# Performance work log

Hardware: AMD Instinct MI355X
Metric: run time of the kernel (lower is better)

## Reference

```python
import jax, jax.numpy as jnp
import numpy as np

N, E, IN, H0, H1 = 50000, 1600000, 64, 64, 128


def _gcn(h, W, b, row, col):
    # PyG GCNConv, add_self_loops=False, unit edge weights:
    # out[col] += d^{-1/2}[row] * d^{-1/2}[col] * (h @ W)[row]; bias added after aggregation
    n = h.shape[0]
    deg = jnp.zeros((n,), h.dtype).at[col].add(jnp.ones((row.shape[0],), h.dtype))
    dinv = jnp.where(deg > 0, jax.lax.rsqrt(jnp.maximum(deg, 1e-12)), 0.0)
    norm = (dinv[row] * dinv[col])[:, None]  # [E,1]
    m = h @ W  # transform before propagate (small GEMM)
    out = jnp.zeros((n, W.shape[1]), h.dtype).at[col].add(norm * m[row])
    return out + b


def _bn(h, g, b):
    # BatchNorm1d training-mode math (biased variance), eps=1e-5
    mu = h.mean(0)
    var = ((h - mu) ** 2).mean(0)
    return g * (h - mu) * jax.lax.rsqrt(var + 1e-5) + b


def _san(h):
    return jnp.nan_to_num(h, nan=0.0, posinf=100.0, neginf=-100.0)


def _slice(x, ei, W0, b0, W1, b1, res1, g0, be0, g1, be1):
    row, col = ei[0], ei[1]
    # layer 0: conv -> bn -> relu -> (dropout=eval identity) -> residual (Identity, 64==64) -> nan_to_num
    h1 = _san(jax.nn.relu(_bn(_gcn(x, W0, b0, row, col), g0, be0)) + x)
    # layer 1 (last): conv -> bn -> residual (Linear proj 64->128, no bias) -> nan_to_num
    h2 = _san(_bn(_gcn(h1, W1, b1, row, col), g1, be1) + h1 @ res1)
    return h2


def setup_inputs() -> dict:
    k = jax.random.split(jax.random.key(0), 16)
    f = lambda kk, sh, s: jax.random.normal(kk, sh, jnp.float32) * s
    return {
        "x": f(k[0], (N, IN), 1.0),
        "edge_index0": jax.random.randint(k[1], (2, E), 0, N),
        "edge_index1": jax.random.randint(k[2], (2, E), 0, N),
        "w0_s0": f(k[3], (IN, H0), 0.1), "b0_s0": jnp.zeros((H0,), jnp.float32),
        "w1_s0": f(k[4], (H0, H1), 0.1), "b1_s0": jnp.zeros((H1,), jnp.float32),
        "res1_s0": f(k[5], (H0, H1), 0.1),
        "w0_s1": f(k[6], (IN, H0), 0.1), "b0_s1": jnp.zeros((H0,), jnp.float32),
        "w1_s1": f(k[7], (H0, H1), 0.1), "b1_s1": jnp.zeros((H1,), jnp.float32),
        "res1_s1": f(k[8], (H0, H1), 0.1),
        "bn_g0": jnp.ones((H0,), jnp.float32), "bn_b0": jnp.zeros((H0,), jnp.float32),
        "bn_g1": jnp.ones((H1,), jnp.float32), "bn_b1": jnp.zeros((H1,), jnp.float32),
        "fc1_w": f(k[9], (2 * H1, H1), 0.1), "fc1_b": jnp.zeros((H1,), jnp.float32),
        "fc2_w": f(k[10], (H1, 2), 0.1), "fc2_b": jnp.zeros((2,), jnp.float32),
    }


def reference(x, edge_index0, edge_index1,
              w0_s0, b0_s0, w1_s0, b1_s0, res1_s0,
              w0_s1, b0_s1, w1_s1, b1_s1, res1_s1,
              bn_g0, bn_b0, bn_g1, bn_b1,
              fc1_w, fc1_b, fc2_w, fc2_b):
    out0 = _slice(x, edge_index0, w0_s0, b0_s0, w1_s0, b1_s0, res1_s0, bn_g0, bn_b0, bn_g1, bn_b1)
    out1 = _slice(x, edge_index1, w0_s1, b0_s1, w1_s1, b1_s1, res1_s1, bn_g0, bn_b0, bn_g1, bn_b1)
    combined = jnp.concatenate([out0, out1], axis=1)  # [N, 2*H1]
    h = jax.nn.relu(combined @ fc1_w + fc1_b)  # dropout is eval-mode identity
    logits = h @ fc2_w + fc2_b
    return logits, jax.nn.softmax(logits, axis=1)
```

## Files before the change

### kernel.cpp

```cpp
#include <hip/hip_runtime.h>
#include <hip/hip_bf16.h>
#include <math.h>


typedef short v8s __attribute__((ext_vector_type(8)));
typedef float f32x4 __attribute__((ext_vector_type(4)));

#define BSTRIDE 10240

__device__ __forceinline__ float sanf(float v) {
    if (v != v) return 0.f;
    if (isinf(v)) return v > 0.f ? 100.f : -100.f;
    return v;
}

__device__ __forceinline__ unsigned short bf16of(float v) {
    __hip_bfloat16 h = __float2bfloat16(v);
    return *(unsigned short*)&h;
}
__device__ __forceinline__ unsigned pack2(float lo, float hi) {
    return (unsigned)bf16of(lo) | ((unsigned)bf16of(hi) << 16);
}
__device__ __forceinline__ float uflo(unsigned u) { return __uint_as_float(u << 16); }
__device__ __forceinline__ float ufhi(unsigned u) { return __uint_as_float(u & 0xFFFF0000u); }
__device__ __forceinline__ float fofbf16(unsigned short u) {
    return __uint_as_float(((unsigned)u) << 16);
}

__device__ __forceinline__ void packone(const float* __restrict__ src, unsigned* __restrict__ dst,
                                        int L, int Khalf, int F) {
    int c = L / Khalf, kp = L - c * Khalf;
    dst[L] = pack2(src[(2 * kp) * F + c], src[(2 * kp + 1) * F + c]);
}

__global__ __launch_bounds__(256) void prep_kernel(const float* __restrict__ w0_0,
                                                   const float* __restrict__ w0_1,
                                                   const float* __restrict__ w1_0,
                                                   const float* __restrict__ w1_1,
                                                   const float* __restrict__ r_0,
                                                   const float* __restrict__ r_1,
                                                   const float* __restrict__ fc1,
                                                   unsigned* __restrict__ wpk,
                                                   int* __restrict__ bcnt,
                                                   float* __restrict__ sums) {
    int gid = blockIdx.x * 256 + threadIdx.x;
    if (gid < 512) bcnt[gid] = 0;
    if (gid < 8192) sums[gid] = 0.f;
    if (gid < 2048)       packone(w0_0, wpk + 0,     gid - 0,     32, 64);
    else if (gid < 4096)  packone(w0_1, wpk + 2048,  gid - 2048,  32, 64);
    else if (gid < 8192)  packone(w1_0, wpk + 4096,  gid - 4096,  32, 128);
    else if (gid < 12288) packone(w1_1, wpk + 8192,  gid - 8192,  32, 128);
    else if (gid < 16384) packone(r_0,  wpk + 12288, gid - 12288, 32, 128);
    else if (gid < 20480) packone(r_1,  wpk + 16384, gid - 16384, 32, 128);
    else if (gid < 36864) packone(fc1,  wpk + 20480, gid - 20480, 128, 128);
}


__global__ __launch_bounds__(512) void kC_bin(const int* __restrict__ ei0,
                                              const int* __restrict__ ei1,
                                              int* __restrict__ bcnt,
                                              unsigned* __restrict__ binned,
                                              int E, int n) {
    __shared__ int cnt[512];
    __shared__ int base[512];
    int t = threadIdx.x;
    cnt[t] = 0;
    int E2 = 2 * E;
    int e0 = blockIdx.x * 8192;
    unsigned pk[16];
    int bk[16];
    __syncthreads();
#pragma unroll
    for (int j = 0; j < 16; ++j) {
        int ge = e0 + t + j * 512;
        bk[j] = -1;
        if (ge < E2) {
            int slice = ge >= E;
            const int* ei = slice ? ei1 : ei0;
            int e = ge - slice * E;
            int col = ei[E + e], row = ei[e];
            int gcol = slice * n + col;
            bk[j] = gcol >> 8;
            pk[j] = (unsigned)row | (((unsigned)gcol & 255u) << 16);
            atomicAdd(&cnt[bk[j]], 1);
        }
    }
    __syncthreads();
    {
        int c = cnt[t];
        base[t] = c ? atomicAdd(&bcnt[t], c) : 0;
    }
    __syncthreads();
    cnt[t] = 0;
    __syncthreads();
#pragma unroll
    for (int j = 0; j < 16; ++j) {
        if (bk[j] >= 0) {
            int loc = atomicAdd(&cnt[bk[j]], 1);
            int off = base[bk[j]] + loc;
            if (off < BSTRIDE) binned[(size_t)bk[j] * BSTRIDE + off] = pk[j];
        }
    }
}

__global__ __launch_bounds__(512) void kD_build(const unsigned* __restrict__ binned,
                                                const int* __restrict__ bcnt,
                                                int* __restrict__ rowptr,
                                                float* __restrict__ dinv,
                                                unsigned short* __restrict__ csr,
                                                int n2, int NB) {
    __shared__ int pref[512];
    __shared__ int cnt[256];
    __shared__ int scn[256];
    __shared__ int cur[256];
    int b = blockIdx.x, t = threadIdx.x;
    pref[t] = (t < NB) ? bcnt[t] : 0;
    __syncthreads();
    for (int off = 1; off < 512; off <<= 1) {
        int u = (t >= off) ? pref[t - off] : 0;
        __syncthreads();
        pref[t] += u;
        __syncthreads();
    }
    int s = (b > 0) ? pref[b - 1] : 0;
    int e = pref[b];
    int m = e - s;
    const unsigned* seg = binned + (size_t)b * BSTRIDE;
    if (t < 256) cnt[t] = 0;
    __syncthreads();
    for (int i = t; i < m; i += 512) atomicAdd(&cnt[(seg[i] >> 16) & 255], 1);
    __syncthreads();
    int v = (t < 256) ? cnt[t] : 0;
    if (t < 256) scn[t] = v;
    __syncthreads();
    for (int off = 1; off < 256; off <<= 1) {
        int u = (t < 256 && t >= off) ? scn[t - off] : 0;
        __syncthreads();
        if (t < 256) scn[t] += u;
        __syncthreads();
    }
    if (t < 256) {
        int excl = scn[t] - v;
        int gcol = b * 256 + t;
        if (gcol < n2) {
            rowptr[gcol] = s + excl;
            dinv[gcol] = v > 0 ? rsqrtf((float)v) : 0.f;
        }
        cur[t] = excl;
    }
    __syncthreads();
    for (int i = t; i < m; i += 512) {
        unsigned p = seg[i];
        int cl = (p >> 16) & 255;
        int pos = s + atomicAdd(&cur[cl], 1);
        csr[pos] = (unsigned short)(p & 0xFFFFu);
    }
    if (b == 0 && t == 0) rowptr[n2] = pref[NB - 1];
}


__global__ __launch_bounds__(256) void prescale_bf(const float* __restrict__ x,
                                                   const float* __restrict__ dinv,
                                                   unsigned short* __restrict__ xsb,
                                                   int n64, int n) {
    int i8 = (blockIdx.x * 256 + threadIdx.x) * 8;
    if (i8 >= n64) return;
    int row = i8 >> 6;
    float4 v0 = *(const float4*)&x[i8];
    float4 v1 = *(const float4*)&x[i8 + 4];
    float d0 = dinv[row], d1 = dinv[n + row];
    uint4 o0, o1;
    o0.x = pack2(v0.x * d0, v0.y * d0); o0.y = pack2(v0.z * d0, v0.w * d0);
    o0.z = pack2(v1.x * d0, v1.y * d0); o0.w = pack2(v1.z * d0, v1.w * d0);
    o1.x = pack2(v0.x * d1, v0.y * d1); o1.y = pack2(v0.z * d1, v0.w * d1);
    o1.z = pack2(v1.x * d1, v1.y * d1); o1.w = pack2(v1.z * d1, v1.w * d1);
    *(uint4*)&xsb[i8] = o0;
    *(uint4*)&xsb[n64 + i8] = o1;
}

#define LOAD8(U, IDX)                                                       \
    do {                                                                    \
        _Pragma("unroll") for (int j = 0; j < 8; ++j) {                     \
            int r = __shfl((IDX), j, 8);                                    \
            (U)[j] = *(const uint4*)&mb[(size_t)r * 64 + l * 8];            \
        }                                                                   \
    } while (0)
#define ZPAD8(U, BB)                                                        \
    do {                                                                    \
        _Pragma("unroll") for (int j = 0; j < 8; ++j)                       \
            if ((BB) + j >= e) { (U)[j].x = 0; (U)[j].y = 0;                \
                                 (U)[j].z = 0; (U)[j].w = 0; }              \
    } while (0)
#define ACC8(U)                                                             \
    do {                                                                    \
        _Pragma("unroll") for (int j = 0; j < 8; ++j) {                     \
            a0 += uflo((U)[j].x); a1 += ufhi((U)[j].x);                     \
            a2 += uflo((U)[j].y); a3 += ufhi((U)[j].y);                     \
            a4 += uflo((U)[j].z); a5 += ufhi((U)[j].z);                     \
            a6 += uflo((U)[j].w); a7 += ufhi((U)[j].w);                     \
        }                                                                   \
    } while (0)

__global__ __launch_bounds__(256) void gatherbf_kernel(const int* __restrict__ rowptr,
                                                       const unsigned short* __restrict__ csr,
                                                       const unsigned short* __restrict__ xsb,
                                                       const float* __restrict__ dinv,
                                                       unsigned short* __restrict__ outb,
                                                       int n) {
    int blk = blockIdx.x;
    int xcd = blk & 7;
    int slice = (xcd >= 4) ? 1 : 0;
    int rank = (blk >> 3) * 4 + (xcd & 3);
    int nodeLocal = rank * 32 + (threadIdx.x >> 3);
    if (nodeLocal >= n) return;
    int node = slice * n + nodeLocal;
    int l = threadIdx.x & 7;
    const unsigned short* mb = xsb + (size_t)slice * n * 64;
    int s = rowptr[node], e = rowptr[node + 1];
    float a0 = 0.f, a1 = 0.f, a2 = 0.f, a3 = 0.f, a4 = 0.f, a5 = 0.f, a6 = 0.f, a7 = 0.f;
    uint4 uA[8], uB[8];
    int b = s;
    if (b + 8 <= e) {
        int ia = csr[b + l];
        LOAD8(uA, ia);
        int bB = b + 8;
        int ib = (bB + l < e) ? (int)csr[bB + l] : 0;
        while (true) {
            bool hasB = (bB < e);
            if (hasB) {
                LOAD8(uB, ib);
                if (bB + 8 > e) ZPAD8(uB, bB);
            }
            int bA2 = bB + 8;
            if (bA2 < e) ia = (bA2 + l < e) ? (int)csr[bA2 + l] : 0;
            ACC8(uA);
            if (!hasB) break;
            bool hasA2 = (bA2 < e);
            if (hasA2) {
                LOAD8(uA, ia);
                if (bA2 + 8 > e) ZPAD8(uA, bA2);
            }
            int bB2 = bA2 + 8;
            if (bB2 < e) ib = (bB2 + l < e) ? (int)csr[bB2 + l] : 0;
            ACC8(uB);
            if (!hasA2) break;
            bB = bB2;
        }
    } else if (b < e) {
        int ia = (b + l < e) ? (int)csr[b + l] : 0;
        LOAD8(uA, ia);
        ZPAD8(uA, b);
        ACC8(uA);
    }
    float d = dinv[node];
    uint4 o;
    o.x = pack2(a0 * d, a1 * d);
    o.y = pack2(a2 * d, a3 * d);
    o.z = pack2(a4 * d, a5 * d);
    o.w = pack2(a6 * d, a7 * d);
    *(uint4*)&outb[(size_t)node * 64 + l * 8] = o;
}


template <int F>
__global__ __launch_bounds__(256) void mfma_gemmb(const unsigned short* __restrict__ Ab,
                                                  const unsigned* __restrict__ WT0,
                                                  const unsigned* __restrict__ WT1,
                                                  unsigned short* __restrict__ Cb,
                                                  float* __restrict__ sums_base,
                                                  int roff, int n) {
    constexpr int NC = F / 16;
    __shared__ float ls[2 * F];
    __shared__ unsigned short stb[64 * F];
    int BPS = (n + 63) >> 6;
    int slice = blockIdx.x >= BPS;
    int sb = blockIdx.x - slice * BPS;
    const unsigned* WT = slice ? WT1 : WT0;
    int row0 = slice * n + sb * 64;
    int rows = min(64, n - sb * 64);
    for (int i = threadIdx.x; i < 2 * F; i += 256) ls[i] = 0.f;
    int w = threadIdx.x >> 6, lane = threadIdx.x & 63, q = lane >> 4, ln = lane & 15;
    const unsigned* A32 = (const unsigned*)Ab;
    size_t arow = (size_t)(row0 + 16 * w + ln) * 32;
    v8s af0 = *(const v8s*)&A32[arow + q * 4];
    v8s af1 = *(const v8s*)&A32[arow + 16 + q * 4];
    f32x4 acc[NC];
#pragma unroll
    for (int ct = 0; ct < NC; ++ct) acc[ct] = {0.f, 0.f, 0.f, 0.f};
#pragma unroll
    for (int ct = 0; ct < NC; ++ct) {
        v8s b0 = *(const v8s*)&WT[(ct * 16 + ln) * 32 + q * 4];
        v8s b1 = *(const v8s*)&WT[(ct * 16 + ln) * 32 + 16 + q * 4];
        acc[ct] = __builtin_amdgcn_mfma_f32_16x16x32_bf16(af0, b0, acc[ct], 0, 0, 0);
        acc[ct] = __builtin_amdgcn_mfma_f32_16x16x32_bf16(af1, b1, acc[ct], 0, 0, 0);
    }
    __syncthreads();
#pragma unroll
    for (int ct = 0; ct < NC; ++ct) {
        float s1 = 0.f, s2 = 0.f;
        int cc = ct * 16 + ln;
#pragma unroll
        for (int i = 0; i < 4; ++i) {
            int r = 16 * w + q * 4 + i;
            stb[r * F + (cc ^ ((r & 7) << 3))] = bf16of(acc[ct][i]);
            if (r < rows) {
                float v = acc[ct][i];
                s1 += v;
                s2 += v * v;
            }
        }
        s1 += __shfl_xor(s1, 16); s1 += __shfl_xor(s1, 32);
        s2 += __shfl_xor(s2, 16); s2 += __shfl_xor(s2, 32);
        if (q == 0) {
            atomicAdd(&ls[cc], s1);
            atomicAdd(&ls[F + cc], s2);
        }
    }
    __syncthreads();
    {
        constexpr int CPT = F / 4;
        int rr = threadIdx.x >> 2, sg = threadIdx.x & 3;
        if (rr < rows) {
            int swz = (rr & 7) << 3;
            int cb = sg * CPT;
            uint4* dst = (uint4*)(Cb + (size_t)(row0 + rr) * F + cb);
#pragma unroll
            for (int jj = 0; jj < CPT / 8; ++jj)
                dst[jj] = *(const uint4*)&stb[rr * F + ((cb + jj * 8) ^ swz)];
        }
    }
    if (threadIdx.x < F) {
        float* dst = sums_base + (blockIdx.x & 7) * 1024 + roff + slice * 2 * F;
        unsafeAtomicAdd(&dst[threadIdx.x], ls[threadIdx.x]);
        unsafeAtomicAdd(&dst[F + threadIdx.x], ls[F + threadIdx.x]);
    }
}

__global__ __launch_bounds__(256) void mfma_apply1(const unsigned short* __restrict__ h1b,
                                                   const unsigned short* __restrict__ Tb,
                                                   const unsigned* __restrict__ RT0,
                                                   const unsigned* __restrict__ RT1,
                                                   const float* __restrict__ sums_base,
                                                   const float* __restrict__ g,
                                                   const float* __restrict__ be,
                                                   unsigned short* __restrict__ comb, int n) {
    __shared__ float st[64 * 128];
    __shared__ float scl[256];
    int BPS = (n + 63) >> 6;
    int slice = blockIdx.x >= BPS;
    int sb = blockIdx.x - slice * BPS;
    const unsigned* WT = slice ? RT1 : RT0;
    int row0 = slice * n + sb * 64;
    int rows = min(64, n - sb * 64);
    int t = threadIdx.x;
    if (t < 128) {
        float s1 = 0.f, s2 = 0.f;
#pragma unroll
        for (int r = 0; r < 8; ++r) {
            const float* src = sums_base + r * 1024 + slice * 256;
            s1 += src[t];
            s2 += src[128 + t];
        }
        float inv_n = 1.0f / (float)n;
        float mu = s1 * inv_n;
        float var = fmaxf(s2 * inv_n - mu * mu, 0.f);
        float scale = g[t] * rsqrtf(var + 1e-5f);
        scl[t] = scale;
        scl[128 + t] = be[t] - mu * scale;
    }
    int w = t >> 6, lane = t & 63, q = lane >> 4, ln = lane & 15;
    const unsigned* A32 = (const unsigned*)h1b;
    size_t arow = (size_t)(row0 + 16 * w + ln) * 32;
    v8s af0 = *(const v8s*)&A32[arow + q * 4];
    v8s af1 = *(const v8s*)&A32[arow + 16 + q * 4];
    f32x4 acc[8];
#pragma unroll
    for (int ct = 0; ct < 8; ++ct) acc[ct] = {0.f, 0.f, 0.f, 0.f};
#pragma unroll
    for (int ct = 0; ct < 8; ++ct) {
        v8s b0 = *(const v8s*)&WT[(ct * 16 + ln) * 32 + q * 4];
        v8s b1 = *(const v8s*)&WT[(ct * 16 + ln) * 32 + 16 + q * 4];
        acc[ct] = __builtin_amdgcn_mfma_f32_16x16x32_bf16(af0, b0, acc[ct], 0, 0, 0);
        acc[ct] = __builtin_amdgcn_mfma_f32_16x16x32_bf16(af1, b1, acc[ct], 0, 0, 0);
    }
#pragma unroll
    for (int ct = 0; ct < 8; ++ct) {
        int cc = ct * 16 + ln;
#pragma unroll
        for (int i = 0; i < 4; ++i) {
            int r = 16 * w + q * 4 + i;
            st[r * 128 + (cc ^ ((r & 7) << 2))] = acc[ct][i];
        }
    }
    __syncthreads();
    int rr = t >> 2, sg = t & 3;
    if (rr >= rows) return;
    int swz = (rr & 7) << 2;
    int rg = row0 + rr;
    const uint4* tbp = (const uint4*)(Tb + (size_t)rg * 128 + sg * 32);
    const float* scb = scl + sg * 32;
    uint4* outp = (uint4*)(comb + (size_t)(rg - slice * n) * 256 + slice * 128 + sg * 32);
#pragma unroll
    for (int jj = 0; jj < 4; ++jj) {
        uint4 tv = tbp[jj];
        int base = sg * 32 + jj * 8;
        float4 a0 = *(const float4*)&st[rr * 128 + (base ^ swz)];
        float4 a1 = *(const float4*)&st[rr * 128 + ((base + 4) ^ swz)];
        float4 s0 = *(const float4*)&scb[jj * 8];
        float4 s1 = *(const float4*)&scb[jj * 8 + 4];
        float4 h0 = *(const float4*)&scb[128 + jj * 8];
        float4 h1v = *(const float4*)&scb[128 + jj * 8 + 4];
        float o0 = sanf(fmaf(uflo(tv.x), s0.x, h0.x) + a0.x);
        float o1 = sanf(fmaf(ufhi(tv.x), s0.y, h0.y) + a0.y);
        float o2 = sanf(fmaf(uflo(tv.y), s0.z, h0.z) + a0.z);
        float o3 = sanf(fmaf(ufhi(tv.y), s0.w, h0.w) + a0.w);
        float o4 = sanf(fmaf(uflo(tv.z), s1.x, h1v.x) + a1.x);
        float o5 = sanf(fmaf(ufhi(tv.z), s1.y, h1v.y) + a1.y);
        float o6 = sanf(fmaf(uflo(tv.w), s1.z, h1v.z) + a1.z);
        float o7 = sanf(fmaf(ufhi(tv.w), s1.w, h1v.w) + a1.w);
        uint4 ov;
        ov.x = pack2(o0, o1);
        ov.y = pack2(o2, o3);
        ov.z = pack2(o4, o5);
        ov.w = pack2(o6, o7);
        outp[jj] = ov;
    }
}

__global__ __launch_bounds__(256) void mfma_head_fc2(const unsigned short* __restrict__ comb,
                                                     const unsigned* __restrict__ FT,
                                                     const float* __restrict__ bias,
                                                     const float* __restrict__ w2,
                                                     const float* __restrict__ b2,
                                                     float* __restrict__ out, int n) {
    int row0 = blockIdx.x * 64;
    int rows = min(64, n - row0);
    int w = threadIdx.x >> 6, lane = threadIdx.x & 63, q = lane >> 4, ln = lane & 15;
    const unsigned* A32 = (const unsigned*)comb;
    size_t arow = (size_t)(row0 + 16 * w + ln) * 128;
    f32x4 acc[8];
#pragma unroll
    for (int ct = 0; ct < 8; ++ct) acc[ct] = {0.f, 0.f, 0.f, 0.f};
#pragma unroll
    for (int kt = 0; kt < 4; ++kt) {
        v8s af0 = *(const v8s*)&A32[arow + kt * 32 + q * 4];
        v8s af1 = *(const v8s*)&A32[arow + kt * 32 + 16 + q * 4];
#pragma unroll
        for (int ct = 0; ct < 8; ++ct) {
            v8s b0 = *(const v8s*)&FT[(ct * 16 + ln) * 128 + kt * 32 + q * 4];
            v8s b1 = *(const v8s*)&FT[(ct * 16 + ln) * 128 + kt * 32 + 16 + q * 4];
            acc[ct] = __builtin_amdgcn_mfma_f32_16x16x32_bf16(af0, b0, acc[ct], 0, 0, 0);
            acc[ct] = __builtin_amdgcn_mfma_f32_16x16x32_bf16(af1, b1, acc[ct], 0, 0, 0);
        }
    }
    float p0[4] = {0.f, 0.f, 0.f, 0.f}, p1[4] = {0.f, 0.f, 0.f, 0.f};
#pragma unroll
    for (int ct = 0; ct < 8; ++ct) {
        int c = ct * 16 + ln;
        float bi = bias[c];
        float w20 = w2[c * 2], w21 = w2[c * 2 + 1];
#pragma unroll
        for (int i = 0; i < 4; ++i) {
            float h = fmaxf(acc[ct][i] + bi, 0.f);
            p0[i] = fmaf(h, w20, p0[i]);
            p1[i] = fmaf(h, w21, p1[i]);
        }
    }
#pragma unroll
    for (int i = 0; i < 4; ++i) {
#pragma unroll
        for (int msk = 1; msk < 16; msk <<= 1) {
            p0[i] += __shfl_xor(p0[i], msk);
            p1[i] += __shfl_xor(p1[i], msk);
        }
    }
    if (ln == 0) {
        float bb0 = b2[0], bb1 = b2[1];
#pragma unroll
        for (int i = 0; i < 4; ++i) {
            int r = 16 * w + q * 4 + i;
            if (r >= rows) continue;
            int R = row0 + r;
            float l0 = p0[i] + bb0, l1 = p1[i] + bb1;
            float mx = fmaxf(l0, l1);
            float e0 = expf(l0 - mx), e1 = expf(l1 - mx);
            float inv = 1.0f / (e0 + e1);
            out[(size_t)R * 2] = l0;
            out[(size_t)R * 2 + 1] = l1;
            out[(size_t)2 * n + R * 2] = e0 * inv;
            out[(size_t)2 * n + R * 2 + 1] = e1 * inv;
        }
    }
}

__global__ __launch_bounds__(256) void apply0_kernel(const unsigned short* __restrict__ t0b,
                                                     const float* __restrict__ x,
                                                     const float* __restrict__ sums_base,
                                                     const float* __restrict__ g,
                                                     const float* __restrict__ be,
                                                     const float* __restrict__ dinv,
                                                     unsigned short* __restrict__ h1b,
                                                     unsigned short* __restrict__ h1sb,
                                                     int n64, int total, int n) {
    __shared__ float sc[256];
    int t = threadIdx.x;
    if (t < 128) {
        int slice = t >> 6, f = t & 63;
        float s1 = 0.f, s2 = 0.f;
#pragma unroll
        for (int r = 0; r < 8; ++r) {
            const float* src = sums_base + r * 1024 + 512 + slice * 128;
            s1 += src[f];
            s2 += src[64 + f];
        }
        float inv_n = 1.0f / (float)n;
        float mu = s1 * inv_n;
        float var = fmaxf(s2 * inv_n - mu * mu, 0.f);
        float scale = g[f] * rsqrtf(var + 1e-5f);
        sc[slice * 128 + f] = scale;
        sc[slice * 128 + 64 + f] = be[f] - mu * scale;
    }
    __syncthreads();
    int i8 = (blockIdx.x * 256 + t) * 8;
    if (i8 >= total) return;
    int slice = i8 >= n64;
    int f0 = i8 & 63;
    const float* scp = sc + slice * 128;
    uint4 tv = *(const uint4*)&t0b[i8];
    const float* xp = x + (i8 - slice * n64);
    float4 x0 = *(const float4*)xp;
    float4 x1 = *(const float4*)(xp + 4);
    float4 s0 = *(const float4*)&scp[f0];
    float4 s1 = *(const float4*)&scp[f0 + 4];
    float4 g0 = *(const float4*)&scp[64 + f0];
    float4 g1 = *(const float4*)&scp[64 + f0 + 4];
    float d = dinv[i8 >> 6];
    float tvv[8] = {uflo(tv.x), ufhi(tv.x), uflo(tv.y), ufhi(tv.y),
                    uflo(tv.z), ufhi(tv.z), uflo(tv.w), ufhi(tv.w)};
    float sa[8] = {s0.x, s0.y, s0.z, s0.w, s1.x, s1.y, s1.z, s1.w};
    float sh[8] = {g0.x, g0.y, g0.z, g0.w, g1.x, g1.y, g1.z, g1.w};
    float xv[8] = {x0.x, x0.y, x0.z, x0.w, x1.x, x1.y, x1.z, x1.w};
    unsigned po[4], ps[4];
#pragma unroll
    for (int j = 0; j < 4; ++j) {
        float a = sanf(fmaxf(fmaf(tvv[2 * j], sa[2 * j], sh[2 * j]), 0.f) + xv[2 * j]);
        float b = sanf(fmaxf(fmaf(tvv[2 * j + 1], sa[2 * j + 1], sh[2 * j + 1]), 0.f) + xv[2 * j + 1]);
        po[j] = pack2(a, b);
        ps[j] = pack2(a * d, b * d);
    }
    *(uint4*)&h1b[i8] = *(uint4*)po;
    *(uint4*)&h1sb[i8] = *(uint4*)ps;
}

static inline int cdiv(int a, int b) { return (a + b - 1) / b; }

extern "C" void kernel_launch(void* const* d_in, const int* in_sizes, int n_in,
                              void* d_out, int out_size, void* d_ws, size_t ws_size,
                              hipStream_t stream) {
    const float* x       = (const float*)d_in[0];
    const int*   ei0     = (const int*)d_in[1];
    const int*   ei1     = (const int*)d_in[2];
    const float* w0_s0   = (const float*)d_in[3];
    const float* w1_s0   = (const float*)d_in[5];
    const float* res1_s0 = (const float*)d_in[7];
    const float* w0_s1   = (const float*)d_in[8];
    const float* w1_s1   = (const float*)d_in[10];
    const float* res1_s1 = (const float*)d_in[12];
    const float* bn_g0   = (const float*)d_in[13];
    const float* bn_b0   = (const float*)d_in[14];
    const float* bn_g1   = (const float*)d_in[15];
    const float* bn_b1   = (const float*)d_in[16];
    const float* fc1_w   = (const float*)d_in[17];
    const float* fc1_b   = (const float*)d_in[18];
    const float* fc2_w   = (const float*)d_in[19];
    const float* fc2_b   = (const float*)d_in[20];
    float* out = (float*)d_out;

    int n = in_sizes[0] / 64;
    int E = in_sizes[1] / 2;
    int n2 = 2 * n, E2 = 2 * E;
    int n64 = n * 64;
    int NB = cdiv(n2, 256);
    int BPS = cdiv(n, 64);
    int GB = 8 * cdiv(cdiv(n, 32), 4);

    float* X1 = (float*)d_ws;
    float* S  = X1 + (size_t)n2 * 64;
    unsigned short* Gb   = (unsigned short*)(S + (size_t)n2 * 64);
    unsigned short* h1b  = Gb + (size_t)n2 * 64;
    unsigned short* comb = h1b + (size_t)n2 * 64;
    unsigned short* xsb  = comb + (size_t)n * 256;
    float* dinv = (float*)(xsb + (size_t)n * 128);
    float* sums = dinv + n2;
    float* scsh = sums + 8192;
    unsigned* wpk = (unsigned*)(scsh + 512);
    unsigned short* csr = (unsigned short*)(wpk + 36864);
    int* rowptr = (int*)(csr + (size_t)E2);
    int* bcnt   = rowptr + (n2 + 1);
    unsigned short* t0b = (unsigned short*)X1;
    unsigned short* Tb  = (unsigned short*)X1;
    unsigned* binned = (unsigned*)comb;
    unsigned short* h1sb = (unsigned short*)S;
    unsigned* w0T0 = wpk + 0,    *w0T1 = wpk + 2048;
    unsigned* w1T0 = wpk + 4096, *w1T1 = wpk + 8192;
    unsigned* rT0  = wpk + 12288,*rT1  = wpk + 16384;
    unsigned* fT   = wpk + 20480;

    prep_kernel<<<144, 256, 0, stream>>>(w0_s0, w0_s1, w1_s0, w1_s1,
                                         res1_s0, res1_s1, fc1_w, wpk, bcnt, sums);
    kC_bin<<<cdiv(E2, 8192), 512, 0, stream>>>(ei0, ei1, bcnt, binned, E, n);
    kD_build<<<NB, 512, 0, stream>>>(binned, bcnt, rowptr, dinv, csr, n2, NB);

    prescale_bf<<<cdiv(n64, 2048), 256, 0, stream>>>(x, dinv, xsb, n64, n);
    gatherbf_kernel<<<GB, 256, 0, stream>>>(rowptr, csr, xsb, dinv, Gb, n);
    mfma_gemmb<64><<<2 * BPS, 256, 0, stream>>>(Gb, w0T0, w0T1, t0b, sums, 512, n);
    apply0_kernel<<<cdiv(2 * n64, 2048), 256, 0, stream>>>(t0b, x, sums, bn_g0, bn_b0,
                                                           dinv, h1b, h1sb, n64, 2 * n64, n);

    gatherbf_kernel<<<GB, 256, 0, stream>>>(rowptr, csr, h1sb, dinv, Gb, n);
    mfma_gemmb<128><<<2 * BPS, 256, 0, stream>>>(Gb, w1T0, w1T1, Tb, sums, 0, n);
    mfma_apply1<<<2 * BPS, 256, 0, stream>>>(h1b, Tb, rT0, rT1, sums, bn_g1, bn_b1, comb, n);

    mfma_head_fc2<<<BPS, 256, 0, stream>>>(comb, fT, fc1_b, fc2_w, fc2_b, out, n);
}
```

Baseline: 353.5 us.

## Fuse prescale into CSR build and fuse apply1 with MLP head

Result: no change. 347.2 us (-1.8%).

```diff
diff --git a/kernel.cpp b/kernel.cpp
--- a/kernel.cpp
+++ b/kernel.cpp
@@ -23,9 +23,6 @@
 }
 __device__ __forceinline__ float uflo(unsigned u) { return __uint_as_float(u << 16); }
 __device__ __forceinline__ float ufhi(unsigned u) { return __uint_as_float(u & 0xFFFF0000u); }
-__device__ __forceinline__ float fofbf16(unsigned short u) {
-    return __uint_as_float(((unsigned)u) << 16);
-}
 
 __device__ __forceinline__ void packone(const float* __restrict__ src, unsigned* __restrict__ dst,
                                         int L, int Khalf, int F) {
@@ -105,15 +102,19 @@
 
 __global__ __launch_bounds__(512) void kD_build(const unsigned* __restrict__ binned,
                                                 const int* __restrict__ bcnt,
+                                                const float* __restrict__ x,
                                                 int* __restrict__ rowptr,
                                                 float* __restrict__ dinv,
                                                 unsigned short* __restrict__ csr,
+                                                unsigned short* __restrict__ xsb,
                                                 int n2, int NB) {
     __shared__ int pref[512];
     __shared__ int cnt[256];
     __shared__ int scn[256];
     __shared__ int cur[256];
+    __shared__ float ds[256];
     int b = blockIdx.x, t = threadIdx.x;
+    int n = n2 >> 1, n64 = n * 64;
     pref[t] = (t < NB) ? bcnt[t] : 0;
     __syncthreads();
     for (int off = 1; off < 512; off <<= 1) {
@@ -142,9 +143,11 @@
     if (t < 256) {
         int excl = scn[t] - v;
         int gcol = b * 256 + t;
+        float dv = v > 0 ? rsqrtf((float)v) : 0.f;
+        ds[t] = dv;
         if (gcol < n2) {
             rowptr[gcol] = s + excl;
-            dinv[gcol] = v > 0 ? rsqrtf((float)v) : 0.f;
+            dinv[gcol] = dv;
         }
         cur[t] = excl;
     }
@@ -155,28 +158,24 @@
         int pos = s + atomicAdd(&cur[cl], 1);
         csr[pos] = (unsigned short)(p & 0xFFFFu);
     }
-    if (b == 0 && t == 0) rowptr[n2] = pref[NB - 1];
-}
-
-
-__global__ __launch_bounds__(256) void prescale_bf(const float* __restrict__ x,
-                                                   const float* __restrict__ dinv,
-                                                   unsigned short* __restrict__ xsb,
-                                                   int n64, int n) {
-    int i8 = (blockIdx.x * 256 + threadIdx.x) * 8;
-    if (i8 >= n64) return;
-    int row = i8 >> 6;
-    float4 v0 = *(const float4*)&x[i8];
-    float4 v1 = *(const float4*)&x[i8 + 4];
-    float d0 = dinv[row], d1 = dinv[n + row];
-    uint4 o0, o1;
-    o0.x = pack2(v0.x * d0, v0.y * d0); o0.y = pack2(v0.z * d0, v0.w * d0);
-    o0.z = pack2(v1.x * d0, v1.y * d0); o0.w = pack2(v1.z * d0, v1.w * d0);
-    o1.x = pack2(v0.x * d1, v0.y * d1); o1.y = pack2(v0.z * d1, v0.w * d1);
-    o1.z = pack2(v1.x * d1, v1.y * d1); o1.w = pack2(v1.z * d1, v1.w * d1);
-    *(uint4*)&xsb[i8] = o0;
-    *(uint4*)&xsb[n64 + i8] = o1;
-}
+    if (b == NB - 1 && t == 0) rowptr[n2] = e;
+    for (int k = t; k < 2048; k += 512) {
+        int gl = k >> 3, segk = k & 7;
+        int gcol = b * 256 + gl;
+        if (gcol >= n2) continue;
+        float d = ds[gl];
+        int slice = gcol >= n;
+        int row = gcol - slice * n;
+        const float* xp = x + (size_t)row * 64 + segk * 8;
+        float4 v0 = *(const float4*)xp;
+        float4 v1 = *(const float4*)(xp + 4);
+        uint4 o;
+        o.x = pack2(v0.x * d, v0.y * d); o.y = pack2(v0.z * d, v0.w * d);
+        o.z = pack2(v1.x * d, v1.y * d); o.w = pack2(v1.z * d, v1.w * d);
+        *(uint4*)&xsb[(size_t)slice * n64 + (size_t)row * 64 + segk * 8] = o;
+    }
+}
+
 
 #define LOAD8(U, IDX)                                                       \
     do {                                                                    \
@@ -336,163 +335,6 @@
     }
 }
 
-__global__ __launch_bounds__(256) void mfma_apply1(const unsigned short* __restrict__ h1b,
-                                                   const unsigned short* __restrict__ Tb,
-                                                   const unsigned* __restrict__ RT0,
-                                                   const unsigned* __restrict__ RT1,
-                                                   const float* __restrict__ sums_base,
-                                                   const float* __restrict__ g,
-                                                   const float* __restrict__ be,
-                                                   unsigned short* __restrict__ comb, int n) {
-    __shared__ float st[64 * 128];
-    __shared__ float scl[256];
-    int BPS = (n + 63) >> 6;
-    int slice = blockIdx.x >= BPS;
-    int sb = blockIdx.x - slice * BPS;
-    const unsigned* WT = slice ? RT1 : RT0;
-    int row0 = slice * n + sb * 64;
-    int rows = min(64, n - sb * 64);
-    int t = threadIdx.x;
-    if (t < 128) {
-        float s1 = 0.f, s2 = 0.f;
-#pragma unroll
-        for (int r = 0; r < 8; ++r) {
-            const float* src = sums_base + r * 1024 + slice * 256;
-            s1 += src[t];
-            s2 += src[128 + t];
-        }
-        float inv_n = 1.0f / (float)n;
-        float mu = s1 * inv_n;
-        float var = fmaxf(s2 * inv_n - mu * mu, 0.f);
-        float scale = g[t] * rsqrtf(var + 1e-5f);
-        scl[t] = scale;
-        scl[128 + t] = be[t] - mu * scale;
-    }
-    int w = t >> 6, lane = t & 63, q = lane >> 4, ln = lane & 15;
-    const unsigned* A32 = (const unsigned*)h1b;
-    size_t arow = (size_t)(row0 + 16 * w + ln) * 32;
-    v8s af0 = *(const v8s*)&A32[arow + q * 4];
-    v8s af1 = *(const v8s*)&A32[arow + 16 + q * 4];
-    f32x4 acc[8];
-#pragma unroll
-    for (int ct = 0; ct < 8; ++ct) acc[ct] = {0.f, 0.f, 0.f, 0.f};
-#pragma unroll
-    for (int ct = 0; ct < 8; ++ct) {
-        v8s b0 = *(const v8s*)&WT[(ct * 16 + ln) * 32 + q * 4];
-        v8s b1 = *(const v8s*)&WT[(ct * 16 + ln) * 32 + 16 + q * 4];
-        acc[ct] = __builtin_amdgcn_mfma_f32_16x16x32_bf16(af0, b0, acc[ct], 0, 0, 0);
-        acc[ct] = __builtin_amdgcn_mfma_f32_16x16x32_bf16(af1, b1, acc[ct], 0, 0, 0);
-    }
-#pragma unroll
-    for (int ct = 0; ct < 8; ++ct) {
-        int cc = ct * 16 + ln;
-#pragma unroll
-        for (int i = 0; i < 4; ++i) {
-            int r = 16 * w + q * 4 + i;
-            st[r * 128 + (cc ^ ((r & 7) << 2))] = acc[ct][i];
-        }
-    }
-    __syncthreads();
-    int rr = t >> 2, sg = t & 3;
-    if (rr >= rows) return;
-    int swz = (rr & 7) << 2;
-    int rg = row0 + rr;
-    const uint4* tbp = (const uint4*)(Tb + (size_t)rg * 128 + sg * 32);
-    const float* scb = scl + sg * 32;
-    uint4* outp = (uint4*)(comb + (size_t)(rg - slice * n) * 256 + slice * 128 + sg * 32);
-#pragma unroll
-    for (int jj = 0; jj < 4; ++jj) {
-        uint4 tv = tbp[jj];
-        int base = sg * 32 + jj * 8;
-        float4 a0 = *(const float4*)&st[rr * 128 + (base ^ swz)];
-        float4 a1 = *(const float4*)&st[rr * 128 + ((base + 4) ^ swz)];
-        float4 s0 = *(const float4*)&scb[jj * 8];
-        float4 s1 = *(const float4*)&scb[jj * 8 + 4];
-        float4 h0 = *(const float4*)&scb[128 + jj * 8];
-        float4 h1v = *(const float4*)&scb[128 + jj * 8 + 4];
-        float o0 = sanf(fmaf(uflo(tv.x), s0.x, h0.x) + a0.x);
-        float o1 = sanf(fmaf(ufhi(tv.x), s0.y, h0.y) + a0.y);
-        float o2 = sanf(fmaf(uflo(tv.y), s0.z, h0.z) + a0.z);
-        float o3 = sanf(fmaf(ufhi(tv.y), s0.w, h0.w) + a0.w);
-        float o4 = sanf(fmaf(uflo(tv.z), s1.x, h1v.x) + a1.x);
-        float o5 = sanf(fmaf(ufhi(tv.z), s1.y, h1v.y) + a1.y);
-        float o6 = sanf(fmaf(uflo(tv.w), s1.z, h1v.z) + a1.z);
-        float o7 = sanf(fmaf(ufhi(tv.w), s1.w, h1v.w) + a1.w);
-        uint4 ov;
-        ov.x = pack2(o0, o1);
-        ov.y = pack2(o2, o3);
-        ov.z = pack2(o4, o5);
-        ov.w = pack2(o6, o7);
-        outp[jj] = ov;
-    }
-}
-
-__global__ __launch_bounds__(256) void mfma_head_fc2(const unsigned short* __restrict__ comb,
-                                                     const unsigned* __restrict__ FT,
-                                                     const float* __restrict__ bias,
-                                                     const float* __restrict__ w2,
-                                                     const float* __restrict__ b2,
-                                                     float* __restrict__ out, int n) {
-    int row0 = blockIdx.x * 64;
-    int rows = min(64, n - row0);
-    int w = threadIdx.x >> 6, lane = threadIdx.x & 63, q = lane >> 4, ln = lane & 15;
-    const unsigned* A32 = (const unsigned*)comb;
-    size_t arow = (size_t)(row0 + 16 * w + ln) * 128;
-    f32x4 acc[8];
-#pragma unroll
-    for (int ct = 0; ct < 8; ++ct) acc[ct] = {0.f, 0.f, 0.f, 0.f};
-#pragma unroll
-    for (int kt = 0; kt < 4; ++kt) {
-        v8s af0 = *(const v8s*)&A32[arow + kt * 32 + q * 4];
-        v8s af1 = *(const v8s*)&A32[arow + kt * 32 + 16 + q * 4];
-#pragma unroll
-        for (int ct = 0; ct < 8; ++ct) {
-            v8s b0 = *(const v8s*)&FT[(ct * 16 + ln) * 128 + kt * 32 + q * 4];
-            v8s b1 = *(const v8s*)&FT[(ct * 16 + ln) * 128 + kt * 32 + 16 + q * 4];
-            acc[ct] = __builtin_amdgcn_mfma_f32_16x16x32_bf16(af0, b0, acc[ct], 0, 0, 0);
-            acc[ct] = __builtin_amdgcn_mfma_f32_16x16x32_bf16(af1, b1, acc[ct], 0, 0, 0);
-        }
-    }
-    float p0[4] = {0.f, 0.f, 0.f, 0.f}, p1[4] = {0.f, 0.f, 0.f, 0.f};
-#pragma unroll
-    for (int ct = 0; ct < 8; ++ct) {
-        int c = ct * 16 + ln;
-        float bi = bias[c];
-        float w20 = w2[c * 2], w21 = w2[c * 2 + 1];
-#pragma unroll
-        for (int i = 0; i < 4; ++i) {
-            float h = fmaxf(acc[ct][i] + bi, 0.f);
-            p0[i] = fmaf(h, w20, p0[i]);
-            p1[i] = fmaf(h, w21, p1[i]);
-        }
-    }
-#pragma unroll
-    for (int i = 0; i < 4; ++i) {
-#pragma unroll
-        for (int msk = 1; msk < 16; msk <<= 1) {
-            p0[i] += __shfl_xor(p0[i], msk);
-            p1[i] += __shfl_xor(p1[i], msk);
-        }
-    }
-    if (ln == 0) {
-        float bb0 = b2[0], bb1 = b2[1];
-#pragma unroll
-        for (int i = 0; i < 4; ++i) {
-            int r = 16 * w + q * 4 + i;
-            if (r >= rows) continue;
-            int R = row0 + r;
-            float l0 = p0[i] + bb0, l1 = p1[i] + bb1;
-            float mx = fmaxf(l0, l1);
-            float e0 = expf(l0 - mx), e1 = expf(l1 - mx);
-            float inv = 1.0f / (e0 + e1);
-            out[(size_t)R * 2] = l0;
-            out[(size_t)R * 2 + 1] = l1;
-            out[(size_t)2 * n + R * 2] = e0 * inv;
-            out[(size_t)2 * n + R * 2 + 1] = e1 * inv;
-        }
-    }
-}
-
 __global__ __launch_bounds__(256) void apply0_kernel(const unsigned short* __restrict__ t0b,
                                                      const float* __restrict__ x,
                                                      const float* __restrict__ sums_base,
@@ -550,6 +392,165 @@
     }
     *(uint4*)&h1b[i8] = *(uint4*)po;
     *(uint4*)&h1sb[i8] = *(uint4*)ps;
+}
+
+__global__ __launch_bounds__(256) void apply1_head(const unsigned short* __restrict__ h1b,
+                                                   const unsigned short* __restrict__ Tb,
+                                                   const unsigned* __restrict__ RT0,
+                                                   const unsigned* __restrict__ RT1,
+                                                   const unsigned* __restrict__ FT,
+                                                   const float* __restrict__ sums_base,
+                                                   const float* __restrict__ g,
+                                                   const float* __restrict__ be,
+                                                   const float* __restrict__ fc1_b,
+                                                   const float* __restrict__ w2,
+                                                   const float* __restrict__ b2,
+                                                   float* __restrict__ out, int n) {
+    __shared__ float st[64 * 128];
+    __shared__ unsigned short cmb[64 * 256];
+    __shared__ float scl[512];
+    int t = threadIdx.x;
+    int row0l = blockIdx.x * 64;
+    int rows = min(64, n - row0l);
+    {
+        int slice = t >> 7, f = t & 127;
+        float s1 = 0.f, s2 = 0.f;
+#pragma unroll
+        for (int r = 0; r < 8; ++r) {
+            const float* src = sums_base + r * 1024 + slice * 256;
+            s1 += src[f];
+            s2 += src[128 + f];
+        }
+        float inv_n = 1.0f / (float)n;
+        float mu = s1 * inv_n;
+        float var = fmaxf(s2 * inv_n - mu * mu, 0.f);
+        float scale = g[f] * rsqrtf(var + 1e-5f);
+        scl[slice * 256 + f] = scale;
+        scl[slice * 256 + 128 + f] = be[f] - mu * scale;
+    }
+    int w = t >> 6, lane = t & 63, q = lane >> 4, ln = lane & 15;
+#pragma unroll
+    for (int slice = 0; slice < 2; ++slice) {
+        const unsigned* WT = slice ? RT1 : RT0;
+        int row0 = slice * n + row0l;
+        const unsigned* A32 = (const unsigned*)h1b;
+        size_t arow = (size_t)(row0 + 16 * w + ln) * 32;
+        v8s af0 = *(const v8s*)&A32[arow + q * 4];
+        v8s af1 = *(const v8s*)&A32[arow + 16 + q * 4];
+        f32x4 acc[8];
+#pragma unroll
+        for (int ct = 0; ct < 8; ++ct) acc[ct] = {0.f, 0.f, 0.f, 0.f};
+#pragma unroll
+        for (int ct = 0; ct < 8; ++ct) {
+            v8s b0 = *(const v8s*)&WT[(ct * 16 + ln) * 32 + q * 4];
+            v8s b1 = *(const v8s*)&WT[(ct * 16 + ln) * 32 + 16 + q * 4];
+            acc[ct] = __builtin_amdgcn_mfma_f32_16x16x32_bf16(af0, b0, acc[ct], 0, 0, 0);
+            acc[ct] = __builtin_amdgcn_mfma_f32_16x16x32_bf16(af1, b1, acc[ct], 0, 0, 0);
+        }
+#pragma unroll
+        for (int ct = 0; ct < 8; ++ct) {
+            int cc = ct * 16 + ln;
+#pragma unroll
+            for (int i = 0; i < 4; ++i) {
+                int r = 16 * w + q * 4 + i;
+                st[r * 128 + (cc ^ ((r & 7) << 2))] = acc[ct][i];
+            }
+        }
+        __syncthreads();
+        int rr = t >> 2, sg = t & 3;
+        if (rr < rows) {
+            int swz = (rr & 7) << 2;
+            int swzB = (rr & 7) << 4;
+            int rg = row0 + rr;
+            const uint4* tbp = (const uint4*)(Tb + (size_t)rg * 128 + sg * 32);
+            const float* scb = scl + slice * 256 + sg * 32;
+            char* cp = (char*)(cmb + rr * 256);
+#pragma unroll
+            for (int jj = 0; jj < 4; ++jj) {
+                uint4 tv = tbp[jj];
+                int base = sg * 32 + jj * 8;
+                float4 a0 = *(const float4*)&st[rr * 128 + (base ^ swz)];
+                float4 a1 = *(const float4*)&st[rr * 128 + ((base + 4) ^ swz)];
+                float4 s0 = *(const float4*)&scb[jj * 8];
+                float4 s1 = *(const float4*)&scb[jj * 8 + 4];
+                float4 h0 = *(const float4*)&scb[128 + jj * 8];
+                float4 h1v = *(const float4*)&scb[128 + jj * 8 + 4];
+                float o0 = sanf(fmaf(uflo(tv.x), s0.x, h0.x) + a0.x);
+                float o1 = sanf(fmaf(ufhi(tv.x), s0.y, h0.y) + a0.y);
+                float o2 = sanf(fmaf(uflo(tv.y), s0.z, h0.z) + a0.z);
+                float o3 = sanf(fmaf(ufhi(tv.y), s0.w, h0.w) + a0.w);
+                float o4 = sanf(fmaf(uflo(tv.z), s1.x, h1v.x) + a1.x);
+                float o5 = sanf(fmaf(ufhi(tv.z), s1.y, h1v.y) + a1.y);
+                float o6 = sanf(fmaf(uflo(tv.w), s1.z, h1v.z) + a1.z);
+                float o7 = sanf(fmaf(ufhi(tv.w), s1.w, h1v.w) + a1.w);
+                uint4 ov;
+                ov.x = pack2(o0, o1);
+                ov.y = pack2(o2, o3);
+                ov.z = pack2(o4, o5);
+                ov.w = pack2(o6, o7);
+                *(uint4*)(cp + ((slice * 256 + sg * 64 + jj * 16) ^ swzB)) = ov;
+            }
+        }
+        __syncthreads();
+    }
+    {
+        int rowLocal = 16 * w + ln;
+        const char* cr = (const char*)(cmb + rowLocal * 256);
+        int swzR = (rowLocal & 7) << 4;
+        f32x4 acc[8];
+#pragma unroll
+        for (int ct = 0; ct < 8; ++ct) acc[ct] = {0.f, 0.f, 0.f, 0.f};
+#pragma unroll
+        for (int kt = 0; kt < 4; ++kt) {
+            v8s af0 = *(const v8s*)(cr + ((kt * 128 + q * 16) ^ swzR));
+            v8s af1 = *(const v8s*)(cr + ((kt * 128 + 64 + q * 16) ^ swzR));
+#pragma unroll
+            for (int ct = 0; ct < 8; ++ct) {
+                v8s b0 = *(const v8s*)&FT[(ct * 16 + ln) * 128 + kt * 32 + q * 4];
+                v8s b1 = *(const v8s*)&FT[(ct * 16 + ln) * 128 + kt * 32 + 16 + q * 4];
+                acc[ct] = __builtin_amdgcn_mfma_f32_16x16x32_bf16(af0, b0, acc[ct], 0, 0, 0);
+                acc[ct] = __builtin_amdgcn_mfma_f32_16x16x32_bf16(af1, b1, acc[ct], 0, 0, 0);
+            }
+        }
+        float p0[4] = {0.f, 0.f, 0.f, 0.f}, p1[4] = {0.f, 0.f, 0.f, 0.f};
+#pragma unroll
+        for (int ct = 0; ct < 8; ++ct) {
+            int c = ct * 16 + ln;
+            float bi = fc1_b[c];
+            float w20 = w2[c * 2], w21 = w2[c * 2 + 1];
+#pragma unroll
+            for (int i = 0; i < 4; ++i) {
+                float h = fmaxf(acc[ct][i] + bi, 0.f);
+                p0[i] = fmaf(h, w20, p0[i]);
+                p1[i] = fmaf(h, w21, p1[i]);
+            }
+        }
+#pragma unroll
+        for (int i = 0; i < 4; ++i) {
+#pragma unroll
+            for (int msk = 1; msk < 16; msk <<= 1) {
+                p0[i] += __shfl_xor(p0[i], msk);
+                p1[i] += __shfl_xor(p1[i], msk);
+            }
+        }
+        if (ln == 0) {
+            float bb0 = b2[0], bb1 = b2[1];
+#pragma unroll
+            for (int i = 0; i < 4; ++i) {
+                int r = 16 * w + q * 4 + i;
+                if (r >= rows) continue;
+                int R = row0l + r;
+                float l0 = p0[i] + bb0, l1 = p1[i] + bb1;
+                float mx = fmaxf(l0, l1);
+                float e0 = expf(l0 - mx), e1 = expf(l1 - mx);
+                float inv = 1.0f / (e0 + e1);
+                out[(size_t)R * 2] = l0;
+                out[(size_t)R * 2 + 1] = l1;
+                out[(size_t)2 * n + R * 2] = e0 * inv;
+                out[(size_t)2 * n + R * 2 + 1] = e1 * inv;
+            }
+        }
+    }
 }
 
 static inline int cdiv(int a, int b) { return (a + b - 1) / b; }
@@ -609,9 +610,8 @@
     prep_kernel<<<144, 256, 0, stream>>>(w0_s0, w0_s1, w1_s0, w1_s1,
                                          res1_s0, res1_s1, fc1_w, wpk, bcnt, sums);
     kC_bin<<<cdiv(E2, 8192), 512, 0, stream>>>(ei0, ei1, bcnt, binned, E, n);
-    kD_build<<<NB, 512, 0, stream>>>(binned, bcnt, rowptr, dinv, csr, n2, NB);
-
-    prescale_bf<<<cdiv(n64, 2048), 256, 0, stream>>>(x, dinv, xsb, n64, n);
+    kD_build<<<NB, 512, 0, stream>>>(binned, bcnt, x, rowptr, dinv, csr, xsb, n2, NB);
+
     gatherbf_kernel<<<GB, 256, 0, stream>>>(rowptr, csr, xsb, dinv, Gb, n);
     mfma_gemmb<64><<<2 * BPS, 256, 0, stream>>>(Gb, w0T0, w0T1, t0b, sums, 512, n);
     apply0_kernel<<<cdiv(2 * n64, 2048), 256, 0, stream>>>(t0b, x, sums, bn_g0, bn_b0,
@@ -619,7 +619,7 @@
 
     gatherbf_kernel<<<GB, 256, 0, stream>>>(rowptr, csr, h1sb, dinv, Gb, n);
     mfma_gemmb<128><<<2 * BPS, 256, 0, stream>>>(Gb, w1T0, w1T1, Tb, sums, 0, n);
-    mfma_apply1<<<2 * BPS, 256, 0, stream>>>(h1b, Tb, rT0, rT1, sums, bn_g1, bn_b1, comb, n);
-
-    mfma_head_fc2<<<BPS, 256, 0, stream>>>(comb, fT, fc1_b, fc2_w, fc2_b, out, n);
-}
+
+    apply1_head<<<BPS, 256, 0, stream>>>(h1b, Tb, rT0, rT1, fT, sums, bn_g1, bn_b1,
+                                         fc1_b, fc2_w, fc2_b, out, n);
+}
```
